# Kernel tuning notes

Measured on AMD Instinct MI355X. Metric: run time of the kernel, lower is better.

The kernel has to match this reference:

```python
import jax, jax.numpy as jnp
import numpy as np

EPS = 1e-8
BETA = 0.02          # bisector-band sharpness
ALPHA_UNION = 8.0    # exp-union strength
W_MIN, W_MAX = 0.005, 0.5
RAW_TEMP = 5.0       # width squash temperature
REL_TEMP = 0.05      # seed-relevance softmax temperature
A_MIN, A_MAX = 0.5, 2.0  # anisotropy eigenvalue range


def setup_inputs() -> dict:
    key = jax.random.key(0)
    k1, k2, k3, k4, k5 = jax.random.split(key, 5)
    N, S = 65536, 32
    return {
        "points_uv": jax.random.uniform(k1, (N, 2), dtype=jnp.float32),
        "seeds_raw": jax.random.uniform(k2, (S, 2), dtype=jnp.float32),
        "w_raw": jax.random.normal(k3, (1,), dtype=jnp.float32),
        "theta": jax.random.normal(k4, (S,), dtype=jnp.float32),
        "a_raw": jax.random.normal(k5, (S,), dtype=jnp.float32),
    }


def _metric_matrices(theta, a_raw):
    # anisotropic 2x2 SPD metrics M_s = R^T diag(a, 1/a) R
    t = jnp.tanh(a_raw)
    a = 0.5 * (A_MAX - A_MIN) * t + 0.5 * (A_MAX + A_MIN)  # (S,)
    c, s = jnp.cos(theta), jnp.sin(theta)
    R = jnp.stack([jnp.stack([c, -s], -1), jnp.stack([s, c], -1)], -2)  # (S,2,2)
    dvec = jnp.stack([a, 1.0 / (a + EPS)], -1)  # (S,2)
    return jnp.einsum("ska,sk,skb->sab", R, dvec, R)  # (S,2,2)


def reference(points_uv, seeds_raw, w_raw, theta, a_raw):
    S = seeds_raw.shape[0]
    # half-thickness around the Voronoi bisector
    w = W_MIN + (W_MAX - W_MIN) * jax.nn.sigmoid(w_raw[0] / RAW_TEMP)
    M = _metric_matrices(theta, a_raw)  # (S,2,2)

    # point-to-seed diffs with periodic wrapping on both u and v
    diff = points_uv[:, None, :] - seeds_raw[None, :, :]  # (N,S,2)
    diff = diff - jnp.round(diff)

    # anisotropic distances d_i(x) = sqrt(diff^T M_i diff)
    d = jnp.sqrt(jnp.einsum("nsa,sab,nsb->ns", diff, M, diff) + EPS)  # (N,S)

    # soft seed relevance -> soft pair weights P_ij (upper triangular, normalized)
    w_soft = jax.nn.softmax(-d / REL_TEMP, axis=1)  # (N,S)
    pair = w_soft[:, :, None] * w_soft[:, None, :]  # (N,S,S)
    mask = jnp.triu(jnp.ones((S, S), dtype=points_uv.dtype), k=1)
    pair = pair * mask
    P = pair / (pair.sum(axis=(1, 2), keepdims=True) + EPS)

    # bisector band: B_ij = sigmoid((w - |d_i - d_j|_smooth) / beta)
    Delta = d[:, :, None] - d[:, None, :]  # (N,S,S)
    abs_smooth = jnp.sqrt(Delta * Delta + EPS)
    B = jax.nn.sigmoid((w - abs_smooth) / BETA)

    # union over i<j pairs: rho = 1 - exp(-alpha * sum S_ij)
    S_sum = jnp.sum(P * B, axis=(1, 2))  # (N,)
    rho = 1.0 - jnp.exp(-ALPHA_UNION * S_sum)
    return rho
```

## Files before the change

kernel.cpp:

```cpp
#include <hip/hip_runtime.h>
#include <math.h>


#define LOG2E 1.4426950408889634f
#define EPSF  1e-8f
#define TSC   4096.0f
#define TAB_N 4160
#define BLOCK 512
#define PPB   64
#define SSTR  40

#define DPP_ADD(X, CTRL)                                                   \
    (X) += __int_as_float(__builtin_amdgcn_mov_dpp(                        \
               __float_as_int(X), (CTRL), 0xf, 0xf, false));

__global__ __launch_bounds__(BLOCK, 8) void voronoi_v11(
    const float* __restrict__ points,
    const float* __restrict__ seeds,
    const float* __restrict__ w_raw,
    const float* __restrict__ theta,
    const float* __restrict__ a_raw,
    float* __restrict__ out,
    int N)
{
    __shared__ float    s_tab[TAB_N];
    __shared__ unsigned s_ii[PPB * SSTR];
    __shared__ float    s_ww[PPB * SSTR];
    __shared__ float    s_su[32], s_sv[32], s_m00[32], s_m01[32], s_m11[32];

    const int t = threadIdx.x;

    const float wr = w_raw[0];
    const float sg = __builtin_amdgcn_rcpf(1.0f + exp2f(wr * (-LOG2E / 5.0f)));
    const float w  = 0.005f + 0.495f * sg;

    if (t < 32) {
        const float x  = a_raw[t];
        const float z  = exp2f(2.0f * LOG2E * x);
        const float th = (z - 1.0f) * __builtin_amdgcn_rcpf(z + 1.0f);
        const float a  = 0.75f * th + 1.25f;
        const float ia = __builtin_amdgcn_rcpf(a + EPSF);
        const float cs = __cosf(theta[t]);
        const float sn = __sinf(theta[t]);
        const float S2 = TSC * TSC;
        s_m00[t] = (a * cs * cs + ia * sn * sn) * S2;
        s_m01[t] = (2.0f * cs * sn * (ia - a)) * S2;
        s_m11[t] = (a * sn * sn + ia * cs * cs) * S2;
        s_su[t]  = seeds[2 * t];
        s_sv[t]  = seeds[2 * t + 1];
    }
    {
        const float kC = (50.0f * LOG2E) / TSC;
        const float kB = -w * (50.0f * LOG2E);
        for (int k = t; k < TAB_N; k += BLOCK) {
            const float y = exp2f(fmaf((float)k, kC, kB));
            s_tab[k] = __builtin_amdgcn_rcpf(1.0f + y);
        }
    }
    __syncthreads();

    const int pb = t >> 3;
    const int g  = t & 7;
    const int s0 = g * 4;
    const int p  = blockIdx.x * PPB + pb;
    if (p >= N) return;

    const float4 su4  = *(const float4*)&s_su[s0];
    const float4 sv4  = *(const float4*)&s_sv[s0];
    const float4 m004 = *(const float4*)&s_m00[s0];
    const float4 m014 = *(const float4*)&s_m01[s0];
    const float4 m114 = *(const float4*)&s_m11[s0];

    const float2 uv = ((const float2*)points)[p];
    const float u = uv.x, v = uv.y;

    const float EPS_Q = 1e-8f * TSC * TSC;
    float4 d4;
#define DIST(SU, SV, M00, M01, M11, OUTD)                                  \
    {                                                                      \
        float du = u - (SU); du -= rintf(du);                              \
        float dv = v - (SV); dv -= rintf(dv);                              \
        float q = fmaf(du * du, (M00),                                     \
                  fmaf(du * dv, (M01),                                     \
                  fmaf(dv * dv, (M11), EPS_Q)));                           \
        (OUTD) = sqrtf(q);                                                 \
    }
    DIST(su4.x, sv4.x, m004.x, m014.x, m114.x, d4.x)
    DIST(su4.y, sv4.y, m004.y, m014.y, m114.y, d4.y)
    DIST(su4.z, sv4.z, m004.z, m014.z, m114.z, d4.z)
    DIST(su4.w, sv4.w, m004.w, m014.w, m114.w, d4.w)

    const float cE = -(20.0f * LOG2E) / TSC;
    float4 e4;
    e4.x = exp2f(d4.x * cE);
    e4.y = exp2f(d4.y * cE);
    e4.z = exp2f(d4.z * cE);
    e4.w = exp2f(d4.w * cE);
    float Z = (e4.x + e4.y) + (e4.z + e4.w);
    DPP_ADD(Z, 0xB1)
    DPP_ADD(Z, 0x4E)
    Z += __shfl_xor(Z, 4, 64);
    const float rcpZ = __builtin_amdgcn_rcpf(Z);
    float4 w4;
    w4.x = e4.x * rcpZ; w4.y = e4.y * rcpZ;
    w4.z = e4.z * rcpZ; w4.w = e4.w * rcpZ;
    float sq = w4.x * w4.x;
    sq = fmaf(w4.y, w4.y, sq);
    sq = fmaf(w4.z, w4.z, sq);
    sq = fmaf(w4.w, w4.w, sq);

    uint4 ii;
    ii.x = ((unsigned)(d4.x + 0.5f)) << 2;
    ii.y = ((unsigned)(d4.y + 0.5f)) << 2;
    ii.z = ((unsigned)(d4.z + 0.5f)) << 2;
    ii.w = ((unsigned)(d4.w + 0.5f)) << 2;

    unsigned* db = &s_ii[pb * SSTR];
    float*    wb = &s_ww[pb * SSTR];
    *(uint4*) (db + s0) = ii;
    *(float4*)(wb + s0) = w4;

    const char* tb = (const char*)s_tab;

#define TBODY(IA, IB, WJ, ACC)                                             \
    {                                                                      \
        const unsigned hi = (IA) > (IB) ? (IA) : (IB);                     \
        const unsigned lo = (IA) > (IB) ? (IB) : (IA);                     \
        const float B = *(const float*)(tb + (hi - lo));                   \
        (ACC) = fmaf((WJ), B, (ACC));                                      \
    }

    float b0, b1, b2, b3;
    b0 = 0.0f; b1 = 0.0f; b2 = 0.0f; b3 = 0.0f;
    TBODY(ii.x, ii.y, w4.y, b0)
    TBODY(ii.x, ii.z, w4.z, b0)
    TBODY(ii.x, ii.w, w4.w, b0)
    TBODY(ii.y, ii.z, w4.z, b1)
    TBODY(ii.y, ii.w, w4.w, b1)
    TBODY(ii.z, ii.w, w4.w, b2)

#define ROT(R)                                                             \
    {                                                                      \
        const int gj = ((g + (R)) & 7) * 4;                                \
        const uint4  ij = *(const uint4*) (db + gj);                       \
        const float4 wj = *(const float4*)(wb + gj);                       \
        TBODY(ii.x, ij.x, wj.x, b0)                                        \
        TBODY(ii.x, ij.y, wj.y, b0)                                        \
        TBODY(ii.x, ij.z, wj.z, b0)                                        \
        TBODY(ii.x, ij.w, wj.w, b0)                                        \
        TBODY(ii.y, ij.x, wj.x, b1)                                        \
        TBODY(ii.y, ij.y, wj.y, b1)                                        \
        TBODY(ii.y, ij.z, wj.z, b1)                                        \
        TBODY(ii.y, ij.w, wj.w, b1)                                        \
        TBODY(ii.z, ij.x, wj.x, b2)                                        \
        TBODY(ii.z, ij.y, wj.y, b2)                                        \
        TBODY(ii.z, ij.z, wj.z, b2)                                        \
        TBODY(ii.z, ij.w, wj.w, b2)                                        \
        TBODY(ii.w, ij.x, wj.x, b3)                                        \
        TBODY(ii.w, ij.y, wj.y, b3)                                        \
        TBODY(ii.w, ij.z, wj.z, b3)                                        \
        TBODY(ii.w, ij.w, wj.w, b3)                                        \
    }
    ROT(1)
    ROT(2)
    ROT(3)

    {
        const int gj = ((g + 4) & 7) * 4;
        const uint4  ij = *(const uint4*) (db + gj);
        const float4 wj = *(const float4*)(wb + gj);
        const bool lo4 = (g < 4);
        const unsigned cA0 = lo4 ? ij.x : ij.z;
        const unsigned cA1 = lo4 ? ij.y : ij.w;
        const float    vA0 = lo4 ? wj.x : wj.z;
        const float    vA1 = lo4 ? wj.y : wj.w;
        const unsigned cB0 = lo4 ? ij.z : ij.x;
        const unsigned cB1 = lo4 ? ij.w : ij.y;
        const float    vB0 = lo4 ? wj.z : wj.x;
        const float    vB1 = lo4 ? wj.w : wj.y;
        TBODY(ii.x, cA0, vA0, b0)
        TBODY(ii.x, cA1, vA1, b0)
        TBODY(ii.y, cA0, vA0, b1)
        TBODY(ii.y, cA1, vA1, b1)
        TBODY(ii.z, cB0, vB0, b2)
        TBODY(ii.z, cB1, vB1, b2)
        TBODY(ii.w, cB0, vB0, b3)
        TBODY(ii.w, cB1, vB1, b3)
    }

    float nb = w4.x * b0;
    nb = fmaf(w4.y, b1, nb);
    nb = fmaf(w4.z, b2, nb);
    nb = fmaf(w4.w, b3, nb);

    DPP_ADD(nb, 0xB1)
    DPP_ADD(sq, 0xB1)
    DPP_ADD(nb, 0x4E)
    DPP_ADD(sq, 0x4E)
    nb += __shfl_xor(nb, 4, 64);
    sq += __shfl_xor(sq, 4, 64);

    const float den   = fmaxf(0.5f * (1.0f - sq), 0.0f) + EPSF;
    const float ratio = nb * __builtin_amdgcn_rcpf(den);
    const float rho   = 1.0f - exp2f(ratio * (-8.0f * LOG2E));
    if (g == 0) out[p] = rho;
}

extern "C" void kernel_launch(void* const* d_in, const int* in_sizes, int n_in,
                              void* d_out, int out_size, void* d_ws, size_t ws_size,
                              hipStream_t stream) {
    const float* points = (const float*)d_in[0];
    const float* seeds  = (const float*)d_in[1];
    const float* w_raw  = (const float*)d_in[2];
    const float* theta  = (const float*)d_in[3];
    const float* a_raw  = (const float*)d_in[4];
    float* out = (float*)d_out;

    const int N = in_sizes[0] / 2;
    const int grid = (N + PPB - 1) / PPB;

    voronoi_v11<<<grid, BLOCK, 0, stream>>>(points, seeds, w_raw, theta, a_raw,
                                            out, N);
}
```

Measured before the change: 15.66 us.

## Shrink sigmoid table to clamped band window, replicate entries per lane, pack indices

Halves the distance quantization scale and builds the sigmoid lookup table only over a window around the band centre. Values outside the window are clamped, since the sigmoid saturates there. Each entry is replicated 8 times so that the 8 lanes of a point group read distinct LDS banks, which is meant to remove bank conflicts on the gather. Seed indices are packed as 16-bit pairs to cut LDS traffic, at the cost of extra clamp and min/max ALU work per lookup and coarser quantization accuracy.

```diff
diff --git a/kernel.cpp b/kernel.cpp
--- a/kernel.cpp
+++ b/kernel.cpp
@@ -4,17 +4,18 @@
 
 #define LOG2E 1.4426950408889634f
 #define EPSF  1e-8f
-#define TSC   4096.0f
-#define TAB_N 4160
+#define TSC   2048.0f
+#define HB    376
+#define SPANM 753
 #define BLOCK 512
 #define PPB   64
-#define SSTR  40
+#define SSTR  52
 
 #define DPP_ADD(X, CTRL)                                                   \
     (X) += __int_as_float(__builtin_amdgcn_mov_dpp(                        \
                __float_as_int(X), (CTRL), 0xf, 0xf, false));
 
-__global__ __launch_bounds__(BLOCK, 8) void voronoi_v11(
+__global__ __launch_bounds__(BLOCK, 8) void voronoi_v15(
     const float* __restrict__ points,
     const float* __restrict__ seeds,
     const float* __restrict__ w_raw,
@@ -23,9 +24,8 @@
     float* __restrict__ out,
     int N)
 {
-    __shared__ float    s_tab[TAB_N];
-    __shared__ unsigned s_ii[PPB * SSTR];
-    __shared__ float    s_ww[PPB * SSTR];
+    __shared__ float    s_tab[SPANM * 8];
+    __shared__ unsigned s_sl[PPB * SSTR];
     __shared__ float    s_su[32], s_sv[32], s_m00[32], s_m01[32], s_m11[32];
 
     const int t = threadIdx.x;
@@ -33,6 +33,10 @@
     const float wr = w_raw[0];
     const float sg = __builtin_amdgcn_rcpf(1.0f + exp2f(wr * (-LOG2E / 5.0f)));
     const float w  = 0.005f + 0.495f * sg;
+
+    const int icent = (int)fmaf(w, TSC, 0.5f);
+    const int T1    = icent > HB ? icent - HB : 0;
+    const int SPAN  = (icent + HB + 1) - T1;
 
     if (t < 32) {
         const float x  = a_raw[t];
@@ -49,13 +53,12 @@
         s_su[t]  = seeds[2 * t];
         s_sv[t]  = seeds[2 * t + 1];
     }
-    {
-        const float kC = (50.0f * LOG2E) / TSC;
-        const float kB = -w * (50.0f * LOG2E);
-        for (int k = t; k < TAB_N; k += BLOCK) {
-            const float y = exp2f(fmaf((float)k, kC, kB));
-            s_tab[k] = __builtin_amdgcn_rcpf(1.0f + y);
-        }
+    for (int k = t; k < SPAN; k += BLOCK) {
+        const float arg = fmaf(-(float)(T1 + k), 50.0f / TSC, 50.0f * w);
+        const float val = __builtin_amdgcn_rcpf(1.0f + exp2f(-arg * LOG2E));
+        float4 v4; v4.x = val; v4.y = val; v4.z = val; v4.w = val;
+        float4* dst = (float4*)&s_tab[k << 3];
+        dst[0] = v4; dst[1] = v4;
     }
     __syncthreads();
 
@@ -64,6 +67,11 @@
     const int s0 = g * 4;
     const int p  = blockIdx.x * PPB + pb;
     if (p >= N) return;
+
+    const int c4   = (t & 7) << 2;
+    const int adjB = c4 - (T1 << 5);
+    const int loA  = c4;
+    const int hiA  = ((SPAN - 1) << 5) + c4;
 
     const float4 su4  = *(const float4*)&s_su[s0];
     const float4 sv4  = *(const float4*)&s_sv[s0];
@@ -109,83 +117,97 @@
     sq = fmaf(w4.z, w4.z, sq);
     sq = fmaf(w4.w, w4.w, sq);
 
-    uint4 ii;
-    ii.x = ((unsigned)(d4.x + 0.5f)) << 2;
-    ii.y = ((unsigned)(d4.y + 0.5f)) << 2;
-    ii.z = ((unsigned)(d4.z + 0.5f)) << 2;
-    ii.w = ((unsigned)(d4.w + 0.5f)) << 2;
-
-    unsigned* db = &s_ii[pb * SSTR];
-    float*    wb = &s_ww[pb * SSTR];
-    *(uint4*) (db + s0) = ii;
-    *(float4*)(wb + s0) = w4;
+    int i0 = (int)(d4.x + 0.5f);
+    int i1 = (int)(d4.y + 0.5f);
+    int i2 = (int)(d4.z + 0.5f);
+    int i3 = (int)(d4.w + 0.5f);
+
+    unsigned* row = &s_sl[pb * SSTR];
+    {
+        uint2 pk;
+        pk.x = (unsigned)i0 | ((unsigned)i1 << 16);
+        pk.y = (unsigned)i2 | ((unsigned)i3 << 16);
+        *(uint2*)(row + 2 * g) = pk;
+        *(float4*)(row + 16 + 4 * g) = w4;
+    }
 
     const char* tb = (const char*)s_tab;
 
-#define TBODY(IA, IB, WJ, ACC)                                             \
+#define TB(IA, IB, WJ, ACC)                                                \
     {                                                                      \
-        const unsigned hi = (IA) > (IB) ? (IA) : (IB);                     \
-        const unsigned lo = (IA) > (IB) ? (IB) : (IA);                     \
-        const float B = *(const float*)(tb + (hi - lo));                   \
+        const int hi = (IA) > (IB) ? (IA) : (IB);                          \
+        const int lo = (IA) > (IB) ? (IB) : (IA);                          \
+        int a = ((hi - lo) << 5) + adjB;                                   \
+        a = a > loA ? a : loA;                                             \
+        a = a < hiA ? a : hiA;                                             \
+        const float B = *(const float*)(tb + a);                           \
         (ACC) = fmaf((WJ), B, (ACC));                                      \
     }
 
     float b0, b1, b2, b3;
     b0 = 0.0f; b1 = 0.0f; b2 = 0.0f; b3 = 0.0f;
-    TBODY(ii.x, ii.y, w4.y, b0)
-    TBODY(ii.x, ii.z, w4.z, b0)
-    TBODY(ii.x, ii.w, w4.w, b0)
-    TBODY(ii.y, ii.z, w4.z, b1)
-    TBODY(ii.y, ii.w, w4.w, b1)
-    TBODY(ii.z, ii.w, w4.w, b2)
+    TB(i0, i1, w4.y, b0)
+    TB(i0, i2, w4.z, b0)
+    TB(i0, i3, w4.w, b0)
+    TB(i1, i2, w4.z, b1)
+    TB(i1, i3, w4.w, b1)
+    TB(i2, i3, w4.w, b2)
 
 #define ROT(R)                                                             \
     {                                                                      \
-        const int gj = ((g + (R)) & 7) * 4;                                \
-        const uint4  ij = *(const uint4*) (db + gj);                       \
-        const float4 wj = *(const float4*)(wb + gj);                       \
-        TBODY(ii.x, ij.x, wj.x, b0)                                        \
-        TBODY(ii.x, ij.y, wj.y, b0)                                        \
-        TBODY(ii.x, ij.z, wj.z, b0)                                        \
-        TBODY(ii.x, ij.w, wj.w, b0)                                        \
-        TBODY(ii.y, ij.x, wj.x, b1)                                        \
-        TBODY(ii.y, ij.y, wj.y, b1)                                        \
-        TBODY(ii.y, ij.z, wj.z, b1)                                        \
-        TBODY(ii.y, ij.w, wj.w, b1)                                        \
-        TBODY(ii.z, ij.x, wj.x, b2)                                        \
-        TBODY(ii.z, ij.y, wj.y, b2)                                        \
-        TBODY(ii.z, ij.z, wj.z, b2)                                        \
-        TBODY(ii.z, ij.w, wj.w, b2)                                        \
-        TBODY(ii.w, ij.x, wj.x, b3)                                        \
-        TBODY(ii.w, ij.y, wj.y, b3)                                        \
-        TBODY(ii.w, ij.z, wj.z, b3)                                        \
-        TBODY(ii.w, ij.w, wj.w, b3)                                        \
+        const int gj = ((g + (R)) & 7);                                    \
+        const uint2  ip = *(const uint2*) (row + 2 * gj);                  \
+        const float4 wj = *(const float4*)(row + 16 + 4 * gj);             \
+        const int j0 = (int)(ip.x & 0xffffu);                              \
+        const int j1 = (int)(ip.x >> 16);                                  \
+        const int j2 = (int)(ip.y & 0xffffu);                              \
+        const int j3 = (int)(ip.y >> 16);                                  \
+        TB(i0, j0, wj.x, b0)                                               \
+        TB(i0, j1, wj.y, b0)                                               \
+        TB(i0, j2, wj.z, b0)                                               \
+        TB(i0, j3, wj.w, b0)                                               \
+        TB(i1, j0, wj.x, b1)                                               \
+        TB(i1, j1, wj.y, b1)                                               \
+        TB(i1, j2, wj.z, b1)                                               \
+        TB(i1, j3, wj.w, b1)                                               \
+        TB(i2, j0, wj.x, b2)                                               \
+        TB(i2, j1, wj.y, b2)                                               \
+        TB(i2, j2, wj.z, b2)                                               \
+        TB(i2, j3, wj.w, b2)                                               \
+        TB(i3, j0, wj.x, b3)                                               \
+        TB(i3, j1, wj.y, b3)                                               \
+        TB(i3, j2, wj.z, b3)                                               \
+        TB(i3, j3, wj.w, b3)                                               \
     }
     ROT(1)
     ROT(2)
     ROT(3)
 
     {
-        const int gj = ((g + 4) & 7) * 4;
-        const uint4  ij = *(const uint4*) (db + gj);
-        const float4 wj = *(const float4*)(wb + gj);
+        const int gj = ((g + 4) & 7);
+        const uint2  ip = *(const uint2*) (row + 2 * gj);
+        const float4 wj = *(const float4*)(row + 16 + 4 * gj);
+        const int j0 = (int)(ip.x & 0xffffu);
+        const int j1 = (int)(ip.x >> 16);
+        const int j2 = (int)(ip.y & 0xffffu);
+        const int j3 = (int)(ip.y >> 16);
         const bool lo4 = (g < 4);
-        const unsigned cA0 = lo4 ? ij.x : ij.z;
-        const unsigned cA1 = lo4 ? ij.y : ij.w;
-        const float    vA0 = lo4 ? wj.x : wj.z;
-        const float    vA1 = lo4 ? wj.y : wj.w;
-        const unsigned cB0 = lo4 ? ij.z : ij.x;
-        const unsigned cB1 = lo4 ? ij.w : ij.y;
-        const float    vB0 = lo4 ? wj.z : wj.x;
-        const float    vB1 = lo4 ? wj.w : wj.y;
-        TBODY(ii.x, cA0, vA0, b0)
-        TBODY(ii.x, cA1, vA1, b0)
-        TBODY(ii.y, cA0, vA0, b1)
-        TBODY(ii.y, cA1, vA1, b1)
-        TBODY(ii.z, cB0, vB0, b2)
-        TBODY(ii.z, cB1, vB1, b2)
-        TBODY(ii.w, cB0, vB0, b3)
-        TBODY(ii.w, cB1, vB1, b3)
+        const int   cA0 = lo4 ? j0 : j2;
+        const int   cA1 = lo4 ? j1 : j3;
+        const float vA0 = lo4 ? wj.x : wj.z;
+        const float vA1 = lo4 ? wj.y : wj.w;
+        const int   cB0 = lo4 ? j2 : j0;
+        const int   cB1 = lo4 ? j3 : j1;
+        const float vB0 = lo4 ? wj.z : wj.x;
+        const float vB1 = lo4 ? wj.w : wj.y;
+        TB(i0, cA0, vA0, b0)
+        TB(i0, cA1, vA1, b0)
+        TB(i1, cA0, vA0, b1)
+        TB(i1, cA1, vA1, b1)
+        TB(i2, cB0, vB0, b2)
+        TB(i2, cB1, vB1, b2)
+        TB(i3, cB0, vB0, b3)
+        TB(i3, cB1, vB1, b3)
     }
 
     float nb = w4.x * b0;
@@ -219,6 +241,6 @@
     const int N = in_sizes[0] / 2;
     const int grid = (N + PPB - 1) / PPB;
 
-    voronoi_v11<<<grid, BLOCK, 0, stream>>>(points, seeds, w_raw, theta, a_raw,
+    voronoi_v15<<<grid, BLOCK, 0, stream>>>(points, seeds, w_raw, theta, a_raw,
                                             out, N);
 }
```

New measurement: 15.53 us. No clear change (-0.9%).
